# Optimization experiments

Measured on AMD Instinct MI355X. Metric: run time of the kernel, lower is better.

Reference implementation:

```python
import jax, jax.numpy as jnp
import numpy as np
from jax import lax

E = 4; D_MODEL = 128; D_FF = 128; DT_RANK = 32; D_STATE = 16
L = 12; PAD = 12  # padding_factor=1.0 -> pad L extra zeros
K_TOP = 6; U = 1e-6; EPS = 1e-5
BATCH = 8; NODES = 307; BN = BATCH * NODES
FREQ_IN = (L + PAD) // 2 + 1 + K_TOP  # 19
FREQ_OUT = L // 2 + 1                 # 7


def setup_inputs() -> dict:
    key = jax.random.key(0)
    ks = jax.random.split(key, 14)
    x = jax.random.normal(ks[0], (BN, L, D_MODEL), jnp.float32)
    graph = jax.random.normal(ks[1], (BATCH, L, D_FF, D_FF), jnp.float32) * (1.0 / D_FF)
    in_w = jax.random.normal(ks[2], (E, 2 * D_FF, D_MODEL), jnp.float32) * 0.05
    in_b = jax.random.normal(ks[3], (E, 2 * D_FF), jnp.float32) * 0.02
    x_w = jax.random.normal(ks[4], (E, DT_RANK + 2 * D_STATE + D_FF, D_FF), jnp.float32) * 0.05
    dt_w = jax.random.uniform(ks[5], (E, D_FF, DT_RANK), jnp.float32,
                              -(DT_RANK ** -0.5), DT_RANK ** -0.5)
    dt_b = -2.0 + 0.1 * jax.random.normal(ks[6], (E, D_FF), jnp.float32)
    A_log = jnp.broadcast_to(jnp.log(jnp.arange(1, D_STATE + 1, dtype=jnp.float32))[None, None, :],
                             (E, 1, D_STATE))
    out_w = jax.random.normal(ks[7], (E, D_MODEL, D_FF), jnp.float32) * 0.05
    out_b = jax.random.normal(ks[8], (E, D_MODEL), jnp.float32) * 0.02
    fw_r = jax.random.normal(ks[9], (E, FREQ_OUT, FREQ_IN), jnp.float32) * (FREQ_IN ** -0.5)
    fw_i = jax.random.normal(ks[10], (E, FREQ_OUT, FREQ_IN), jnp.float32) * (FREQ_IN ** -0.5)
    norm_w = jnp.ones((E, D_MODEL), jnp.float32)
    blk_w = jnp.full((E,), 0.5, jnp.float32)
    blk_b = jnp.full((E,), 0.5, jnp.float32)
    return dict(x=x, graph=graph, in_w=in_w, in_b=in_b, x_w=x_w, dt_w=dt_w, dt_b=dt_b,
                A_log=A_log, out_w=out_w, out_b=out_b, fw_r=fw_r, fw_i=fw_i,
                norm_w=norm_w, blk_w=blk_w, blk_b=blk_b)


def _rmsnorm(x, w):
    return x * lax.rsqrt(jnp.mean(x * x, axis=-1, keepdims=True) + EPS) * w


def _mamba_block(x, graph, in_w, in_b, x_w, dt_w, dt_b, A_log, out_w, out_b, fw_r, fw_i):
    bn, Ls, d = x.shape
    # --- FFT frequency gating ---
    x_padded = jnp.concatenate([x, jnp.zeros((bn, PAD, d), x.dtype)], axis=1)
    fp = jnp.fft.rfft(x_padded, axis=1)          # [bn, 13, d] complex
    f = jnp.fft.rfft(x, axis=1)                  # [bn, 7, d] complex
    sq_adj = (f.real + U) ** 2 + (f.imag + U) ** 2
    fs = -jnp.sort(-sq_adj, axis=1)[:, :K_TOP]   # top-K along freq dim, descending
    cat = jnp.concatenate([fp, fs.astype(fp.dtype)], axis=1)  # [bn, 19, d]
    W = lax.complex(fw_r, fw_i)                  # [7, 19]
    freq_proj = jnp.einsum('bkd,ok->bod', cat, W)  # [bn, 7, d]
    wf = jax.nn.softmax(freq_proj.real ** 2 + freq_proj.imag ** 2, axis=2)
    x_freq = jnp.fft.irfft(wf * f, axis=1)       # [bn, 12, d] (n = 2*(7-1))
    # --- input projection ---
    xz = x @ in_w.T + in_b
    xs, z = jnp.split(xz, 2, axis=-1)
    xs = jax.nn.silu(xs)
    # --- SSM ---
    A = -jnp.exp(A_log.astype(jnp.float32))      # [1, d_state]
    dbcd = xs @ x_w.T
    delta, B, C, Dp = jnp.split(dbcd, [DT_RANK, DT_RANK + D_STATE, DT_RANK + 2 * D_STATE], axis=-1)
    delta = jax.nn.softplus(delta @ dt_w.T + dt_b)  # [bn, L, d_ff]
    # graph mixing over nodes: bn = batch * n
    batch = graph.shape[0]
    delta = delta.reshape(batch, -1, Ls, D_FF)
    delta = jnp.einsum('bnsd,bsda->bnsa', delta, graph).reshape(bn, Ls, D_FF)
    deltaA = jnp.exp(delta[..., None] * A)             # [bn, L, d_ff, d_state]
    BX = delta[..., None] * B[:, :, None, :] * xs[..., None]
    dA_t = jnp.moveaxis(deltaA, 1, 0)
    bx_t = jnp.moveaxis(BX, 1, 0)

    def step(h, ab):
        dA, bx = ab
        h = dA * h + bx
        return h, h

    h0 = jnp.zeros((bn, D_FF, D_STATE), xs.dtype)
    _, hs = lax.scan(step, h0, (dA_t, bx_t))
    hs = jnp.moveaxis(hs, 0, 1)                        # [bn, L, d_ff, d_state]
    y = jnp.einsum('blds,bls->bld', hs, C) + Dp * xs
    # --- gate + output ---
    out = y * jax.nn.silu(z) * x_freq
    return out @ out_w.T + out_b


def reference(x, graph, in_w, in_b, x_w, dt_w, dt_b, A_log, out_w, out_b,
              fw_r, fw_i, norm_w, blk_w, blk_b):
    for i in range(E):
        xn = _rmsnorm(x, norm_w[i])
        out = _mamba_block(xn, graph, in_w[i], in_b[i], x_w[i], dt_w[i], dt_b[i],
                           A_log[i], out_w[i], out_b[i], fw_r[i], fw_i[i])
        out = blk_w[i] * out + blk_b[i]
        x = x + out  # dropout is identity in eval
    return jax.nn.silu(x)
```

## Files before the change

kernel.cpp:

```cpp
#include <hip/hip_runtime.h>
#include <math.h>

#define BN    2456
#define LSEQ  12
#define DM    128
#define NODES 307
#define MROWS 29472

typedef __bf16 bfx8 __attribute__((ext_vector_type(8)));
typedef float  f32x4 __attribute__((ext_vector_type(4)));

#define MFMA16(a, b, c) __builtin_amdgcn_mfma_f32_16x16x32_bf16(a, b, c, 0, 0, 0)

__device__ __forceinline__ float fsilu(float v)     { return v / (1.0f + __expf(-v)); }
__device__ __forceinline__ float fsoftplus(float x) { return fmaxf(x, 0.f) + __logf(1.0f + __expf(-fabsf(x))); }

__global__ __launch_bounds__(256)
void k_convert(const float* __restrict__ in_w, const float* __restrict__ x_w,
               const float* __restrict__ out_w, const float* __restrict__ dt_w,
               const float* __restrict__ graph,
               __bf16* __restrict__ in_w_bf, __bf16* __restrict__ x_w_bf,
               __bf16* __restrict__ out_w_bf, __bf16* __restrict__ dtw_bf,
               __bf16* __restrict__ graphT_bf) {
    int idx = blockIdx.x * 256 + threadIdx.x;
    if (idx < 131072) { in_w_bf[idx] = (__bf16)in_w[idx]; return; }
    idx -= 131072;
    if (idx < 98304) { x_w_bf[idx] = (__bf16)x_w[idx]; return; }
    idx -= 98304;
    if (idx < 65536) { out_w_bf[idx] = (__bf16)out_w[idx]; return; }
    idx -= 65536;
    if (idx < 65536) { dtw_bf[idx] = (__bf16)dt_w[idx]; return; }
    idx -= 65536;
    if (idx < 1572864) {
        int bl = idx >> 14, r = idx & 16383;
        int d = r >> 7, a = r & 127;
        graphT_bf[(size_t)bl * 16384 + a * 128 + d] = (__bf16)graph[idx];
    }
}

template <int N>
__device__ __forceinline__ void red_sum128(float* v, float* sred, int tid) {
#pragma unroll
    for (int off = 32; off; off >>= 1)
#pragma unroll
        for (int i = 0; i < N; ++i) v[i] += __shfl_xor(v[i], off, 64);
    if ((tid & 63) == 0) {
#pragma unroll
        for (int i = 0; i < N; ++i) sred[(tid >> 6) * N + i] = v[i];
    }
    __syncthreads();
#pragma unroll
    for (int i = 0; i < N; ++i) v[i] = sred[i] + sred[N + i];
    __syncthreads();
}

template <int N>
__device__ __forceinline__ void red_max128(float* v, float* sred, int tid) {
#pragma unroll
    for (int off = 32; off; off >>= 1)
#pragma unroll
        for (int i = 0; i < N; ++i) v[i] = fmaxf(v[i], __shfl_xor(v[i], off, 64));
    if ((tid & 63) == 0) {
#pragma unroll
        for (int i = 0; i < N; ++i) sred[(tid >> 6) * N + i] = v[i];
    }
    __syncthreads();
#pragma unroll
    for (int i = 0; i < N; ++i) v[i] = fmaxf(sred[i], sred[N + i]);
    __syncthreads();
}

__global__ __launch_bounds__(128)
void k_freq(const float* __restrict__ xcur, const float* __restrict__ norm_w,
            const float* __restrict__ fw_r, const float* __restrict__ fw_i,
            __bf16* __restrict__ xn_bf, __bf16* __restrict__ xfq_bf, int e) {
    __shared__ float s_c[24], s_s[24], s_wr[133], s_wi[133];
    __shared__ float sred[24];
    const int row = blockIdx.x, tid = threadIdx.x;
    const int b = row / NODES, n = row - b * NODES;

    if (tid < 24) {
        float sv, cv;
        __sincosf(6.283185307179586f * (float)tid / 24.0f, &sv, &cv);
        s_c[tid] = cv; s_s[tid] = sv;
    }
    for (int i = tid; i < 133; i += 128) { s_wr[i] = fw_r[e * 133 + i]; s_wi[i] = fw_i[e * 133 + i]; }

    const float* xp = xcur + (size_t)row * 1536 + tid;
    float xv[12], v[12];
#pragma unroll
    for (int l = 0; l < 12; ++l) { xv[l] = xp[l * 128]; v[l] = xv[l] * xv[l]; }
    __syncthreads();
    red_sum128<12>(v, sred, tid);

    const float nrmw = norm_w[e * DM + tid];
    float xnr[12];
#pragma unroll
    for (int l = 0; l < 12; ++l)
        xnr[l] = xv[l] * rsqrtf(v[l] * (1.0f / 128.0f) + 1e-5f) * nrmw;

#pragma unroll
    for (int l = 0; l < 12; ++l)
        xn_bf[((size_t)(b * 12 + l) * NODES + n) * 128 + tid] = (__bf16)xnr[l];

    float fpr[13], fpi[13];
#pragma unroll
    for (int k = 0; k < 13; ++k) { fpr[k] = 0.f; fpi[k] = 0.f; }
#pragma unroll
    for (int l = 0; l < 12; ++l) {
#pragma unroll
        for (int k = 0; k < 13; ++k) {
            const int t = (k * l) % 24;
            fpr[k] += xnr[l] * s_c[t];
            fpi[k] -= xnr[l] * s_s[t];
        }
    }

    float a7[7];
#pragma unroll
    for (int o2 = 0; o2 < 7; ++o2) {
        float ar = fpr[2 * o2] + 1e-6f, ai = fpi[2 * o2] + 1e-6f;
        a7[o2] = ar * ar + ai * ai;
    }
#pragma unroll
    for (int pss = 0; pss < 6; ++pss)
#pragma unroll
        for (int j = 0; j < 6; ++j) {
            float hi = fmaxf(a7[j], a7[j + 1]);
            float lo = fminf(a7[j], a7[j + 1]);
            a7[j] = hi; a7[j + 1] = lo;
        }

    float p7[7];
#pragma unroll
    for (int o2 = 0; o2 < 7; ++o2) {
        float pr = 0.f, pi = 0.f;
#pragma unroll
        for (int k = 0; k < 13; ++k) {
            const float wr = s_wr[o2 * 19 + k], wi = s_wi[o2 * 19 + k];
            pr += fpr[k] * wr - fpi[k] * wi;
            pi += fpr[k] * wi + fpi[k] * wr;
        }
#pragma unroll
        for (int k = 0; k < 6; ++k) {
            const float wr = s_wr[o2 * 19 + 13 + k], wi = s_wi[o2 * 19 + 13 + k];
            pr += a7[k] * wr;
            pi += a7[k] * wi;
        }
        p7[o2] = pr * pr + pi * pi;
    }

    float m7[7], ex[7], sm[7];
#pragma unroll
    for (int o2 = 0; o2 < 7; ++o2) m7[o2] = p7[o2];
    red_max128<7>(m7, sred, tid);
#pragma unroll
    for (int o2 = 0; o2 < 7; ++o2) { ex[o2] = __expf(p7[o2] - m7[o2]); sm[o2] = ex[o2]; }
    red_sum128<7>(sm, sred, tid);

    float gr[7], gi[7];
#pragma unroll
    for (int o2 = 0; o2 < 7; ++o2) {
        const float wf = ex[o2] / sm[o2];
        gr[o2] = wf * fpr[2 * o2];
        gi[o2] = wf * fpi[2 * o2];
    }

#pragma unroll
    for (int l = 0; l < 12; ++l) {
        float val = gr[0] + ((l & 1) ? -gr[6] : gr[6]);
#pragma unroll
        for (int o2 = 1; o2 < 6; ++o2) {
            const int t = (2 * o2 * l) % 24;
            val += 2.0f * (gr[o2] * s_c[t] - gi[o2] * s_s[t]);
        }
        xfq_bf[((size_t)(b * 12 + l) * NODES + n) * 128 + tid] = (__bf16)(val * (1.0f / 12.0f));
    }
}

__global__ __launch_bounds__(256)
void k_fused(const __bf16* __restrict__ xn_bf, const __bf16* __restrict__ in_w_bf,
             const float* __restrict__ in_b, const __bf16* __restrict__ x_w_bf,
             const __bf16* __restrict__ dtw_bf, const float* __restrict__ dt_b,
             const __bf16* __restrict__ graphT_bf,
             __bf16* __restrict__ xs_bf, __bf16* __restrict__ sz_bf,
             float* __restrict__ bcf32, __bf16* __restrict__ dpf,
             __bf16* __restrict__ dmix_bf, int e) {
    __shared__ __bf16 sxs[16 * 136];
    __shared__ __bf16 sdelta[16 * 136];
    __shared__ __bf16 sdel32[16 * 40];
    const int bl = blockIdx.x;
    const int n0 = blockIdx.y * 16;
    const int tid = threadIdx.x;
    const int wave = tid >> 6, lane = tid & 63;
    const int lm = lane & 15, lq = lane >> 4;
    const size_t rowbase = (size_t)bl * NODES + n0;

    const __bf16* Wi = in_w_bf + (size_t)e * 256 * 128;
    const size_t arow = (size_t)bl * NODES + min(n0 + lm, NODES - 1);
    bfx8 af[4];
#pragma unroll
    for (int kc = 0; kc < 4; ++kc)
        af[kc] = *(const bfx8*)(xn_bf + arow * 128 + kc * 32 + lq * 8);

    f32x4 acc[4];
#pragma unroll
    for (int nt = 0; nt < 4; ++nt) acc[nt] = (f32x4){0.f, 0.f, 0.f, 0.f};
#pragma unroll
    for (int kc = 0; kc < 4; ++kc) {
        const int kb = kc * 32 + lq * 8;
#pragma unroll
        for (int ntl = 0; ntl < 4; ++ntl) {
            bfx8 b = *(const bfx8*)(Wi + (size_t)(wave * 64 + ntl * 16 + lm) * 128 + kb);
            acc[ntl] = MFMA16(af[kc], b, acc[ntl]);
        }
    }
#pragma unroll
    for (int ntl = 0; ntl < 4; ++ntl) {
        const int col = wave * 64 + ntl * 16 + lm;
        const float bias = in_b[e * 256 + col];
#pragma unroll
        for (int r = 0; r < 4; ++r) {
            const int node = lq * 4 + r;
            const float v = fsilu(acc[ntl][r] + bias);
            const int ok = (n0 + node) < NODES;
            if (col < 128) {
                sxs[node * 136 + col] = (__bf16)v;
                if (ok) xs_bf[(rowbase + node) * 128 + col] = (__bf16)v;
            } else if (ok) {
                sz_bf[(rowbase + node) * 128 + (col - 128)] = (__bf16)v;
            }
        }
    }
    __syncthreads();

    const __bf16* Wx = x_w_bf + (size_t)e * 192 * 128;
    bfx8 ax[4];
#pragma unroll
    for (int kc = 0; kc < 4; ++kc)
        ax[kc] = *(const bfx8*)(sxs + lm * 136 + kc * 32 + lq * 8);

    f32x4 xacc[3];
#pragma unroll
    for (int nt = 0; nt < 3; ++nt) xacc[nt] = (f32x4){0.f, 0.f, 0.f, 0.f};
#pragma unroll
    for (int kc = 0; kc < 4; ++kc) {
        const int kb = kc * 32 + lq * 8;
#pragma unroll
        for (int ntl = 0; ntl < 3; ++ntl) {
            bfx8 b = *(const bfx8*)(Wx + (size_t)((wave * 3 + ntl) * 16 + lm) * 128 + kb);
            xacc[ntl] = MFMA16(ax[kc], b, xacc[ntl]);
        }
    }
#pragma unroll
    for (int ntl = 0; ntl < 3; ++ntl) {
        const int col = (wave * 3 + ntl) * 16 + lm;
#pragma unroll
        for (int r = 0; r < 4; ++r) {
            const int node = lq * 4 + r;
            const float v = xacc[ntl][r];
            const int ok = (n0 + node) < NODES;
            if (col < 32) sdel32[node * 40 + col] = (__bf16)v;
            else if (col < 64) { if (ok) bcf32[(rowbase + node) * 32 + (col - 32)] = v; }
            else if (ok) dpf[(rowbase + node) * 128 + (col - 64)] = (__bf16)v;
        }
    }
    __syncthreads();

    const __bf16* DW = dtw_bf + (size_t)e * 128 * 32;
    bfx8 ad = *(const bfx8*)(sdel32 + lm * 40 + lq * 8);
    const f32x4 z4 = {0.f, 0.f, 0.f, 0.f};
#pragma unroll
    for (int ntl = 0; ntl < 2; ++ntl) {
        const int nt = wave * 2 + ntl;
        bfx8 b = *(const bfx8*)(DW + (size_t)(nt * 16 + lm) * 32 + lq * 8);
        f32x4 dacc = MFMA16(ad, b, z4);
        const int col = nt * 16 + lm;
        const float bias = dt_b[e * 128 + col];
#pragma unroll
        for (int r = 0; r < 4; ++r) {
            const int node = lq * 4 + r;
            sdelta[node * 136 + col] = (__bf16)fsoftplus(dacc[r] + bias);
        }
    }
    __syncthreads();

    const __bf16* Gp = graphT_bf + (size_t)bl * 16384;
    bfx8 ag[4];
#pragma unroll
    for (int kc = 0; kc < 4; ++kc)
        ag[kc] = *(const bfx8*)(sdelta + lm * 136 + kc * 32 + lq * 8);

#pragma unroll
    for (int ntl = 0; ntl < 2; ++ntl) {
        const int nt = wave * 2 + ntl;
        f32x4 gacc = z4;
#pragma unroll
        for (int kc = 0; kc < 4; ++kc) {
            const int kb = kc * 32 + lq * 8;
            bfx8 b = *(const bfx8*)(Gp + (size_t)(nt * 16 + lm) * 128 + kb);
            gacc = MFMA16(ag[kc], b, gacc);
        }
        const int col = nt * 16 + lm;
#pragma unroll
        for (int r = 0; r < 4; ++r) {
            const int node = lq * 4 + r;
            if ((n0 + node) < NODES)
                dmix_bf[(rowbase + node) * 128 + col] = (__bf16)gacc[r];
        }
    }
}

__global__ __launch_bounds__(128)
void k_scanout(const __bf16* __restrict__ dmix_bf, const __bf16* __restrict__ xs_bf,
               const __bf16* __restrict__ sz_bf, const __bf16* __restrict__ xfq_bf,
               const float* __restrict__ bcf32, const __bf16* __restrict__ dpf,
               const float* __restrict__ A_log, const __bf16* __restrict__ out_w_bf,
               const float* __restrict__ out_b, const float* __restrict__ blk_w,
               const float* __restrict__ blk_b, const float* __restrict__ xprev,
               float* __restrict__ xout, int e, int last) {
    __shared__ __bf16 s_out[16 * 136];
    __shared__ float sBC[384];
    const int row = blockIdx.x, tid = threadIdx.x;
    const int b = row / NODES, n = row - b * NODES;
    for (int i = tid; i < 384; i += 128) {
        const int l = i >> 5, s = i & 31;
        sBC[i] = bcf32[((size_t)(b * 12 + l) * NODES + n) * 32 + s];
    }
    float As[16];
#pragma unroll
    for (int s = 0; s < 16; ++s) As[s] = -__expf(A_log[e * 16 + s]);
#pragma unroll
    for (int r = 12; r < 16; ++r) s_out[r * 136 + tid] = (__bf16)0.f;
    __syncthreads();

    float h[16];
#pragma unroll
    for (int s = 0; s < 16; ++s) h[s] = 0.f;
#pragma unroll
    for (int l = 0; l < 12; ++l) {
        const size_t base = ((size_t)(b * 12 + l) * NODES + n) * 128 + tid;
        const float dl = (float)dmix_bf[base];
        const float xv = (float)xs_bf[base];
        const float Dp = (float)dpf[base];
        const float dlx = dl * xv;
        float y = 0.f;
#pragma unroll
        for (int s = 0; s < 16; ++s) {
            h[s] = __expf(dl * As[s]) * h[s] + sBC[l * 32 + s] * dlx;
            y += h[s] * sBC[l * 32 + 16 + s];
        }
        y += Dp * xv;
        const float g = y * (float)sz_bf[base] * (float)xfq_bf[base];
        s_out[l * 136 + tid] = (__bf16)g;
    }
    __syncthreads();

    const int wave = tid >> 6, lane = tid & 63;
    const int lm = lane & 15, lq = lane >> 4;
    const __bf16* Wo = out_w_bf + (size_t)e * 16384;
    bfx8 a[4];
#pragma unroll
    for (int kc = 0; kc < 4; ++kc)
        a[kc] = *(const bfx8*)(s_out + lm * 136 + kc * 32 + lq * 8);

    f32x4 acc[4];
#pragma unroll
    for (int nt = 0; nt < 4; ++nt) acc[nt] = (f32x4){0.f, 0.f, 0.f, 0.f};
#pragma unroll
    for (int kc = 0; kc < 4; ++kc) {
        const int kb = kc * 32 + lq * 8;
#pragma unroll
        for (int nt = 0; nt < 4; ++nt) {
            bfx8 b = *(const bfx8*)(Wo + (size_t)(wave * 64 + nt * 16 + lm) * 128 + kb);
            acc[nt] = MFMA16(a[kc], b, acc[nt]);
        }
    }

    const float bw = blk_w[e], bb = blk_b[e];
#pragma unroll
    for (int nt = 0; nt < 4; ++nt) {
        const int col = wave * 64 + nt * 16 + lm;
        const float ob = out_b[e * 128 + col];
#pragma unroll
        for (int r = 0; r < 4; ++r) {
            const int m = lq * 4 + r;
            if (m < 12) {
                const size_t gi = ((size_t)row * 12 + m) * 128 + col;
                float v = bw * (acc[nt][r] + ob) + bb + xprev[gi];
                if (last) v = fsilu(v);
                xout[gi] = v;
            }
        }
    }
}

extern "C" void kernel_launch(void* const* d_in, const int* in_sizes, int n_in,
                              void* d_out, int out_size, void* d_ws, size_t ws_size,
                              hipStream_t stream) {
    (void)in_sizes; (void)n_in; (void)out_size; (void)ws_size;
    const float* x_in   = (const float*)d_in[0];
    const float* graph  = (const float*)d_in[1];
    const float* in_w   = (const float*)d_in[2];
    const float* in_b   = (const float*)d_in[3];
    const float* x_w    = (const float*)d_in[4];
    const float* dt_w   = (const float*)d_in[5];
    const float* dt_b   = (const float*)d_in[6];
    const float* A_log  = (const float*)d_in[7];
    const float* out_w  = (const float*)d_in[8];
    const float* out_b  = (const float*)d_in[9];
    const float* fw_r   = (const float*)d_in[10];
    const float* fw_i   = (const float*)d_in[11];
    const float* norm_w = (const float*)d_in[12];
    const float* blk_w  = (const float*)d_in[13];
    const float* blk_b  = (const float*)d_in[14];
    float* out = (float*)d_out;

    float* ws = (float*)d_ws;
    size_t o = 0;
    __bf16* in_w_bf   = (__bf16*)(ws + o); o += 131072 / 2;
    __bf16* x_w_bf    = (__bf16*)(ws + o); o += 98304 / 2;
    __bf16* out_w_bf  = (__bf16*)(ws + o); o += 65536 / 2;
    __bf16* dtw_bf    = (__bf16*)(ws + o); o += 65536 / 2;
    __bf16* graphT_bf = (__bf16*)(ws + o); o += 1572864 / 2;
    const size_t NE = (size_t)MROWS * 128;
    __bf16* xn_bf    = (__bf16*)(ws + o); o += NE / 2;
    __bf16* xfq_bf   = (__bf16*)(ws + o); o += NE / 2;
    __bf16* xs_bf    = (__bf16*)(ws + o); o += NE / 2;
    __bf16* sz_bf    = (__bf16*)(ws + o); o += NE / 2;
    __bf16* dpf      = (__bf16*)(ws + o); o += NE / 2;
    __bf16* dmix_bf  = (__bf16*)(ws + o); o += NE / 2;
    float*  bcf32    = ws + o;            o += (size_t)MROWS * 32;

    hipLaunchKernelGGL(k_convert, dim3(7552), dim3(256), 0, stream,
                       in_w, x_w, out_w, dt_w, graph,
                       in_w_bf, x_w_bf, out_w_bf, dtw_bf, graphT_bf);

    for (int e = 0; e < 4; ++e) {
        const float* xcur = (e == 0) ? x_in : (const float*)out;
        const int last = (e == 3) ? 1 : 0;
        hipLaunchKernelGGL(k_freq, dim3(BN), dim3(128), 0, stream,
                           xcur, norm_w, fw_r, fw_i, xn_bf, xfq_bf, e);
        hipLaunchKernelGGL(k_fused, dim3(96, 20), dim3(256), 0, stream,
                           xn_bf, in_w_bf, in_b, x_w_bf, dtw_bf, dt_b, graphT_bf,
                           xs_bf, sz_bf, bcf32, dpf, dmix_bf, e);
        hipLaunchKernelGGL(k_scanout, dim3(BN), dim3(128), 0, stream,
                           dmix_bf, xs_bf, sz_bf, xfq_bf, bcf32, dpf, A_log,
                           out_w_bf, out_b, blk_w, blk_b, xcur, out, e, last);
    }
}
```

Baseline: 465.4 us.

## Fuse RMSNorm and frequency gating into consumers and pre-swizzle weights into MFMA layout

Removes the separate k_freq kernel. RMSNorm is now computed inside k_fused straight from the fp32 activations. The FFT gating is recomputed inside k_scanout, so the xn and xfq bf16 intermediates are no longer written to or read from global memory. Weights and the graph are converted once into an MFMA-fragment-ordered layout, so each lane loads contiguous 16-byte fragments, and they are prefetched early in k_fused. The cost is more register pressure and duplicated RMSNorm work, since both kernels now read xcur in fp32.

```diff
diff --git a/kernel.cpp b/kernel.cpp
--- a/kernel.cpp
+++ b/kernel.cpp
@@ -17,24 +17,55 @@
 
 __global__ __launch_bounds__(256)
 void k_convert(const float* __restrict__ in_w, const float* __restrict__ x_w,
-               const float* __restrict__ out_w, const float* __restrict__ dt_w,
+               const float* __restrict__ dt_w, const float* __restrict__ out_w,
                const float* __restrict__ graph,
-               __bf16* __restrict__ in_w_bf, __bf16* __restrict__ x_w_bf,
-               __bf16* __restrict__ out_w_bf, __bf16* __restrict__ dtw_bf,
-               __bf16* __restrict__ graphT_bf) {
+               __bf16* __restrict__ in_w_sw, __bf16* __restrict__ x_w_sw,
+               __bf16* __restrict__ dtw_sw, __bf16* __restrict__ out_w_sw,
+               __bf16* __restrict__ graph_sw) {
     int idx = blockIdx.x * 256 + threadIdx.x;
-    if (idx < 131072) { in_w_bf[idx] = (__bf16)in_w[idx]; return; }
+    if (idx < 131072) {
+        int o = idx;
+        int e = o >> 15, r = o & 32767;
+        int frag = r >> 9, lane = (r >> 3) & 63, j = r & 7;
+        int nt = frag >> 2, kc = frag & 3, lm = lane & 15, lq = lane >> 4;
+        in_w_sw[o] = (__bf16)in_w[e * 32768 + (nt * 16 + lm) * 128 + kc * 32 + lq * 8 + j];
+        return;
+    }
     idx -= 131072;
-    if (idx < 98304) { x_w_bf[idx] = (__bf16)x_w[idx]; return; }
+    if (idx < 98304) {
+        int o = idx;
+        int e = o / 24576, r = o - e * 24576;
+        int frag = r >> 9, lane = (r >> 3) & 63, j = r & 7;
+        int nt = frag >> 2, kc = frag & 3, lm = lane & 15, lq = lane >> 4;
+        x_w_sw[o] = (__bf16)x_w[e * 24576 + (nt * 16 + lm) * 128 + kc * 32 + lq * 8 + j];
+        return;
+    }
     idx -= 98304;
-    if (idx < 65536) { out_w_bf[idx] = (__bf16)out_w[idx]; return; }
-    idx -= 65536;
-    if (idx < 65536) { dtw_bf[idx] = (__bf16)dt_w[idx]; return; }
+    if (idx < 16384) {
+        int o = idx;
+        int e = o >> 12, r = o & 4095;
+        int nt = r >> 9, lane = (r >> 3) & 63, j = r & 7;
+        int lm = lane & 15, lq = lane >> 4;
+        dtw_sw[o] = (__bf16)dt_w[e * 4096 + (nt * 16 + lm) * 32 + lq * 8 + j];
+        return;
+    }
+    idx -= 16384;
+    if (idx < 65536) {
+        int o = idx;
+        int e = o >> 14, r = o & 16383;
+        int frag = r >> 9, lane = (r >> 3) & 63, j = r & 7;
+        int f = frag >> 2, kc = frag & 3, lm = lane & 15, lq = lane >> 4;
+        out_w_sw[o] = (__bf16)out_w[e * 16384 + (f * 16 + lm) * 128 + kc * 32 + lq * 8 + j];
+        return;
+    }
     idx -= 65536;
     if (idx < 1572864) {
-        int bl = idx >> 14, r = idx & 16383;
-        int d = r >> 7, a = r & 127;
-        graphT_bf[(size_t)bl * 16384 + a * 128 + d] = (__bf16)graph[idx];
+        int o = idx;
+        int bl = o >> 14, r = o & 16383;
+        int frag = r >> 9, lane = (r >> 3) & 63, j = r & 7;
+        int nt = frag >> 2, kc = frag & 3, lm = lane & 15, lq = lane >> 4;
+        int a = nt * 16 + lm, d = kc * 32 + lq * 8 + j;
+        graph_sw[o] = (__bf16)graph[(size_t)bl * 16384 + d * 128 + a];
     }
 }
 
@@ -70,119 +101,11 @@
     __syncthreads();
 }
 
-__global__ __launch_bounds__(128)
-void k_freq(const float* __restrict__ xcur, const float* __restrict__ norm_w,
-            const float* __restrict__ fw_r, const float* __restrict__ fw_i,
-            __bf16* __restrict__ xn_bf, __bf16* __restrict__ xfq_bf, int e) {
-    __shared__ float s_c[24], s_s[24], s_wr[133], s_wi[133];
-    __shared__ float sred[24];
-    const int row = blockIdx.x, tid = threadIdx.x;
-    const int b = row / NODES, n = row - b * NODES;
-
-    if (tid < 24) {
-        float sv, cv;
-        __sincosf(6.283185307179586f * (float)tid / 24.0f, &sv, &cv);
-        s_c[tid] = cv; s_s[tid] = sv;
-    }
-    for (int i = tid; i < 133; i += 128) { s_wr[i] = fw_r[e * 133 + i]; s_wi[i] = fw_i[e * 133 + i]; }
-
-    const float* xp = xcur + (size_t)row * 1536 + tid;
-    float xv[12], v[12];
-#pragma unroll
-    for (int l = 0; l < 12; ++l) { xv[l] = xp[l * 128]; v[l] = xv[l] * xv[l]; }
-    __syncthreads();
-    red_sum128<12>(v, sred, tid);
-
-    const float nrmw = norm_w[e * DM + tid];
-    float xnr[12];
-#pragma unroll
-    for (int l = 0; l < 12; ++l)
-        xnr[l] = xv[l] * rsqrtf(v[l] * (1.0f / 128.0f) + 1e-5f) * nrmw;
-
-#pragma unroll
-    for (int l = 0; l < 12; ++l)
-        xn_bf[((size_t)(b * 12 + l) * NODES + n) * 128 + tid] = (__bf16)xnr[l];
-
-    float fpr[13], fpi[13];
-#pragma unroll
-    for (int k = 0; k < 13; ++k) { fpr[k] = 0.f; fpi[k] = 0.f; }
-#pragma unroll
-    for (int l = 0; l < 12; ++l) {
-#pragma unroll
-        for (int k = 0; k < 13; ++k) {
-            const int t = (k * l) % 24;
-            fpr[k] += xnr[l] * s_c[t];
-            fpi[k] -= xnr[l] * s_s[t];
-        }
-    }
-
-    float a7[7];
-#pragma unroll
-    for (int o2 = 0; o2 < 7; ++o2) {
-        float ar = fpr[2 * o2] + 1e-6f, ai = fpi[2 * o2] + 1e-6f;
-        a7[o2] = ar * ar + ai * ai;
-    }
-#pragma unroll
-    for (int pss = 0; pss < 6; ++pss)
-#pragma unroll
-        for (int j = 0; j < 6; ++j) {
-            float hi = fmaxf(a7[j], a7[j + 1]);
-            float lo = fminf(a7[j], a7[j + 1]);
-            a7[j] = hi; a7[j + 1] = lo;
-        }
-
-    float p7[7];
-#pragma unroll
-    for (int o2 = 0; o2 < 7; ++o2) {
-        float pr = 0.f, pi = 0.f;
-#pragma unroll
-        for (int k = 0; k < 13; ++k) {
-            const float wr = s_wr[o2 * 19 + k], wi = s_wi[o2 * 19 + k];
-            pr += fpr[k] * wr - fpi[k] * wi;
-            pi += fpr[k] * wi + fpi[k] * wr;
-        }
-#pragma unroll
-        for (int k = 0; k < 6; ++k) {
-            const float wr = s_wr[o2 * 19 + 13 + k], wi = s_wi[o2 * 19 + 13 + k];
-            pr += a7[k] * wr;
-            pi += a7[k] * wi;
-        }
-        p7[o2] = pr * pr + pi * pi;
-    }
-
-    float m7[7], ex[7], sm[7];
-#pragma unroll
-    for (int o2 = 0; o2 < 7; ++o2) m7[o2] = p7[o2];
-    red_max128<7>(m7, sred, tid);
-#pragma unroll
-    for (int o2 = 0; o2 < 7; ++o2) { ex[o2] = __expf(p7[o2] - m7[o2]); sm[o2] = ex[o2]; }
-    red_sum128<7>(sm, sred, tid);
-
-    float gr[7], gi[7];
-#pragma unroll
-    for (int o2 = 0; o2 < 7; ++o2) {
-        const float wf = ex[o2] / sm[o2];
-        gr[o2] = wf * fpr[2 * o2];
-        gi[o2] = wf * fpi[2 * o2];
-    }
-
-#pragma unroll
-    for (int l = 0; l < 12; ++l) {
-        float val = gr[0] + ((l & 1) ? -gr[6] : gr[6]);
-#pragma unroll
-        for (int o2 = 1; o2 < 6; ++o2) {
-            const int t = (2 * o2 * l) % 24;
-            val += 2.0f * (gr[o2] * s_c[t] - gi[o2] * s_s[t]);
-        }
-        xfq_bf[((size_t)(b * 12 + l) * NODES + n) * 128 + tid] = (__bf16)(val * (1.0f / 12.0f));
-    }
-}
-
 __global__ __launch_bounds__(256)
-void k_fused(const __bf16* __restrict__ xn_bf, const __bf16* __restrict__ in_w_bf,
-             const float* __restrict__ in_b, const __bf16* __restrict__ x_w_bf,
-             const __bf16* __restrict__ dtw_bf, const float* __restrict__ dt_b,
-             const __bf16* __restrict__ graphT_bf,
+void k_fused(const float* __restrict__ xcur, const float* __restrict__ norm_w,
+             const __bf16* __restrict__ WiSw, const float* __restrict__ in_b,
+             const __bf16* __restrict__ WxSw, const __bf16* __restrict__ DWSw,
+             const float* __restrict__ dt_b, const __bf16* __restrict__ GSw,
              __bf16* __restrict__ xs_bf, __bf16* __restrict__ sz_bf,
              float* __restrict__ bcf32, __bf16* __restrict__ dpf,
              __bf16* __restrict__ dmix_bf, int e) {
@@ -194,27 +117,79 @@
     const int tid = threadIdx.x;
     const int wave = tid >> 6, lane = tid & 63;
     const int lm = lane & 15, lq = lane >> 4;
+    const int b = bl / 12, l = bl - b * 12;
     const size_t rowbase = (size_t)bl * NODES + n0;
 
-    const __bf16* Wi = in_w_bf + (size_t)e * 256 * 128;
-    const size_t arow = (size_t)bl * NODES + min(n0 + lm, NODES - 1);
+    const int nodeA = min(n0 + lm, NODES - 1);
+    const float* xrow = xcur + ((size_t)(b * NODES + nodeA) * 12 + l) * 128 + lq * 8;
+    float xv[4][8];
+#pragma unroll
+    for (int kc = 0; kc < 4; ++kc) {
+        float4 p0 = *(const float4*)(xrow + kc * 32);
+        float4 p1 = *(const float4*)(xrow + kc * 32 + 4);
+        xv[kc][0] = p0.x; xv[kc][1] = p0.y; xv[kc][2] = p0.z; xv[kc][3] = p0.w;
+        xv[kc][4] = p1.x; xv[kc][5] = p1.y; xv[kc][6] = p1.z; xv[kc][7] = p1.w;
+    }
+    float ss = 0.f;
+#pragma unroll
+    for (int kc = 0; kc < 4; ++kc)
+#pragma unroll
+        for (int j = 0; j < 8; ++j) ss += xv[kc][j] * xv[kc][j];
+    ss += __shfl_xor(ss, 16, 64);
+    ss += __shfl_xor(ss, 32, 64);
+    const float rms = rsqrtf(ss * (1.0f / 128.0f) + 1e-5f);
+
     bfx8 af[4];
-#pragma unroll
-    for (int kc = 0; kc < 4; ++kc)
-        af[kc] = *(const bfx8*)(xn_bf + arow * 128 + kc * 32 + lq * 8);
-
+    const float* nwp = norm_w + e * DM + lq * 8;
+#pragma unroll
+    for (int kc = 0; kc < 4; ++kc) {
+        float4 w0 = *(const float4*)(nwp + kc * 32);
+        float4 w1 = *(const float4*)(nwp + kc * 32 + 4);
+        af[kc][0] = (__bf16)(xv[kc][0] * rms * w0.x);
+        af[kc][1] = (__bf16)(xv[kc][1] * rms * w0.y);
+        af[kc][2] = (__bf16)(xv[kc][2] * rms * w0.z);
+        af[kc][3] = (__bf16)(xv[kc][3] * rms * w0.w);
+        af[kc][4] = (__bf16)(xv[kc][4] * rms * w1.x);
+        af[kc][5] = (__bf16)(xv[kc][5] * rms * w1.y);
+        af[kc][6] = (__bf16)(xv[kc][6] * rms * w1.z);
+        af[kc][7] = (__bf16)(xv[kc][7] * rms * w1.w);
+    }
+
+    const __bf16* WxP = WxSw + (size_t)e * 24576;
+    bfx8 b2[3][4];
+#pragma unroll
+    for (int ntl = 0; ntl < 3; ++ntl)
+#pragma unroll
+        for (int kc = 0; kc < 4; ++kc)
+            b2[ntl][kc] = *(const bfx8*)(WxP + (((wave * 3 + ntl) * 4 + kc) * 64 + lane) * 8);
+
+    const __bf16* WiP = WiSw + (size_t)e * 32768;
     f32x4 acc[4];
 #pragma unroll
     for (int nt = 0; nt < 4; ++nt) acc[nt] = (f32x4){0.f, 0.f, 0.f, 0.f};
 #pragma unroll
-    for (int kc = 0; kc < 4; ++kc) {
-        const int kb = kc * 32 + lq * 8;
-#pragma unroll
-        for (int ntl = 0; ntl < 4; ++ntl) {
-            bfx8 b = *(const bfx8*)(Wi + (size_t)(wave * 64 + ntl * 16 + lm) * 128 + kb);
-            acc[ntl] = MFMA16(af[kc], b, acc[ntl]);
-        }
-    }
+    for (int ntl = 0; ntl < 4; ++ntl) {
+        const int nt = wave * 4 + ntl;
+#pragma unroll
+        for (int kc = 0; kc < 4; ++kc) {
+            bfx8 bb = *(const bfx8*)(WiP + ((nt * 4 + kc) * 64 + lane) * 8);
+            acc[ntl] = MFMA16(af[kc], bb, acc[ntl]);
+        }
+    }
+
+    const __bf16* DWp = DWSw + (size_t)e * 4096;
+    bfx8 b3[2];
+#pragma unroll
+    for (int ntl = 0; ntl < 2; ++ntl)
+        b3[ntl] = *(const bfx8*)(DWp + ((wave * 2 + ntl) * 64 + lane) * 8);
+    const __bf16* Gp = GSw + (size_t)bl * 16384;
+    bfx8 b4[2][4];
+#pragma unroll
+    for (int ntl = 0; ntl < 2; ++ntl)
+#pragma unroll
+        for (int kc = 0; kc < 4; ++kc)
+            b4[ntl][kc] = *(const bfx8*)(Gp + (((wave * 2 + ntl) * 4 + kc) * 64 + lane) * 8);
+
 #pragma unroll
     for (int ntl = 0; ntl < 4; ++ntl) {
         const int col = wave * 64 + ntl * 16 + lm;
@@ -234,7 +209,6 @@
     }
     __syncthreads();
 
-    const __bf16* Wx = x_w_bf + (size_t)e * 192 * 128;
     bfx8 ax[4];
 #pragma unroll
     for (int kc = 0; kc < 4; ++kc)
@@ -244,14 +218,11 @@
 #pragma unroll
     for (int nt = 0; nt < 3; ++nt) xacc[nt] = (f32x4){0.f, 0.f, 0.f, 0.f};
 #pragma unroll
-    for (int kc = 0; kc < 4; ++kc) {
-        const int kb = kc * 32 + lq * 8;
-#pragma unroll
-        for (int ntl = 0; ntl < 3; ++ntl) {
-            bfx8 b = *(const bfx8*)(Wx + (size_t)((wave * 3 + ntl) * 16 + lm) * 128 + kb);
-            xacc[ntl] = MFMA16(ax[kc], b, xacc[ntl]);
-        }
-    }
+    for (int ntl = 0; ntl < 3; ++ntl)
+#pragma unroll
+        for (int kc = 0; kc < 4; ++kc)
+            xacc[ntl] = MFMA16(ax[kc], b2[ntl][kc], xacc[ntl]);
+
 #pragma unroll
     for (int ntl = 0; ntl < 3; ++ntl) {
         const int col = (wave * 3 + ntl) * 16 + lm;
@@ -267,15 +238,12 @@
     }
     __syncthreads();
 
-    const __bf16* DW = dtw_bf + (size_t)e * 128 * 32;
     bfx8 ad = *(const bfx8*)(sdel32 + lm * 40 + lq * 8);
     const f32x4 z4 = {0.f, 0.f, 0.f, 0.f};
 #pragma unroll
     for (int ntl = 0; ntl < 2; ++ntl) {
-        const int nt = wave * 2 + ntl;
-        bfx8 b = *(const bfx8*)(DW + (size_t)(nt * 16 + lm) * 32 + lq * 8);
-        f32x4 dacc = MFMA16(ad, b, z4);
-        const int col = nt * 16 + lm;
+        f32x4 dacc = MFMA16(ad, b3[ntl], z4);
+        const int col = (wave * 2 + ntl) * 16 + lm;
         const float bias = dt_b[e * 128 + col];
 #pragma unroll
         for (int r = 0; r < 4; ++r) {
@@ -285,7 +253,6 @@
     }
     __syncthreads();
 
-    const __bf16* Gp = graphT_bf + (size_t)bl * 16384;
     bfx8 ag[4];
 #pragma unroll
     for (int kc = 0; kc < 4; ++kc)
@@ -293,15 +260,11 @@
 
 #pragma unroll
     for (int ntl = 0; ntl < 2; ++ntl) {
-        const int nt = wave * 2 + ntl;
         f32x4 gacc = z4;
 #pragma unroll
-        for (int kc = 0; kc < 4; ++kc) {
-            const int kb = kc * 32 + lq * 8;
-            bfx8 b = *(const bfx8*)(Gp + (size_t)(nt * 16 + lm) * 128 + kb);
-            gacc = MFMA16(ag[kc], b, gacc);
-        }
-        const int col = nt * 16 + lm;
+        for (int kc = 0; kc < 4; ++kc)
+            gacc = MFMA16(ag[kc], b4[ntl][kc], gacc);
+        const int col = (wave * 2 + ntl) * 16 + lm;
 #pragma unroll
         for (int r = 0; r < 4; ++r) {
             const int node = lq * 4 + r;
@@ -312,28 +275,133 @@
 }
 
 __global__ __launch_bounds__(128)
-void k_scanout(const __bf16* __restrict__ dmix_bf, const __bf16* __restrict__ xs_bf,
-               const __bf16* __restrict__ sz_bf, const __bf16* __restrict__ xfq_bf,
-               const float* __restrict__ bcf32, const __bf16* __restrict__ dpf,
-               const float* __restrict__ A_log, const __bf16* __restrict__ out_w_bf,
-               const float* __restrict__ out_b, const float* __restrict__ blk_w,
-               const float* __restrict__ blk_b, const float* __restrict__ xprev,
+void k_scanout(const float* __restrict__ xcur, const float* __restrict__ norm_w,
+               const float* __restrict__ fw_r, const float* __restrict__ fw_i,
+               const __bf16* __restrict__ dmix_bf, const __bf16* __restrict__ xs_bf,
+               const __bf16* __restrict__ sz_bf, const float* __restrict__ bcf32,
+               const __bf16* __restrict__ dpf, const float* __restrict__ A_log,
+               const __bf16* __restrict__ WoSw, const float* __restrict__ out_b,
+               const float* __restrict__ blk_w, const float* __restrict__ blk_b,
                float* __restrict__ xout, int e, int last) {
+    __shared__ float s_c[24], s_s[24], s_wr[133], s_wi[133];
+    __shared__ float sred[24];
     __shared__ __bf16 s_out[16 * 136];
     __shared__ float sBC[384];
     const int row = blockIdx.x, tid = threadIdx.x;
     const int b = row / NODES, n = row - b * NODES;
-    for (int i = tid; i < 384; i += 128) {
-        const int l = i >> 5, s = i & 31;
-        sBC[i] = bcf32[((size_t)(b * 12 + l) * NODES + n) * 32 + s];
-    }
+
+    float bcreg[3];
+#pragma unroll
+    for (int i = 0; i < 3; ++i) {
+        const int ii = tid + i * 128;
+        const int l = ii >> 5, s = ii & 31;
+        bcreg[i] = bcf32[((size_t)(b * 12 + l) * NODES + n) * 32 + s];
+    }
+
+    if (tid < 24) {
+        float sv, cv;
+        __sincosf(6.283185307179586f * (float)tid / 24.0f, &sv, &cv);
+        s_c[tid] = cv; s_s[tid] = sv;
+    }
+    for (int i = tid; i < 133; i += 128) { s_wr[i] = fw_r[e * 133 + i]; s_wi[i] = fw_i[e * 133 + i]; }
+
+    const float* xp = xcur + (size_t)row * 1536 + tid;
+    float xvf[12], v[12];
+#pragma unroll
+    for (int l = 0; l < 12; ++l) { xvf[l] = xp[l * 128]; v[l] = xvf[l] * xvf[l]; }
+    __syncthreads();
+    red_sum128<12>(v, sred, tid);
+
+    const float nrmw = norm_w[e * DM + tid];
+    float xnr[12];
+#pragma unroll
+    for (int l = 0; l < 12; ++l)
+        xnr[l] = xvf[l] * rsqrtf(v[l] * (1.0f / 128.0f) + 1e-5f) * nrmw;
+
+    float fpr[13], fpi[13];
+#pragma unroll
+    for (int k = 0; k < 13; ++k) { fpr[k] = 0.f; fpi[k] = 0.f; }
+#pragma unroll
+    for (int l = 0; l < 12; ++l) {
+#pragma unroll
+        for (int k = 0; k < 13; ++k) {
+            const int t = (k * l) % 24;
+            fpr[k] += xnr[l] * s_c[t];
+            fpi[k] -= xnr[l] * s_s[t];
+        }
+    }
+
+    float a7[7];
+#pragma unroll
+    for (int o2 = 0; o2 < 7; ++o2) {
+        float ar = fpr[2 * o2] + 1e-6f, ai = fpi[2 * o2] + 1e-6f;
+        a7[o2] = ar * ar + ai * ai;
+    }
+#pragma unroll
+    for (int pss = 0; pss < 6; ++pss)
+#pragma unroll
+        for (int j = 0; j < 6; ++j) {
+            float hi = fmaxf(a7[j], a7[j + 1]);
+            float lo = fminf(a7[j], a7[j + 1]);
+            a7[j] = hi; a7[j + 1] = lo;
+        }
+
+    float p7[7];
+#pragma unroll
+    for (int o2 = 0; o2 < 7; ++o2) {
+        float pr = 0.f, pi = 0.f;
+#pragma unroll
+        for (int k = 0; k < 13; ++k) {
+            const float wr = s_wr[o2 * 19 + k], wi = s_wi[o2 * 19 + k];
+            pr += fpr[k] * wr - fpi[k] * wi;
+            pi += fpr[k] * wi + fpi[k] * wr;
+        }
+#pragma unroll
+        for (int k = 0; k < 6; ++k) {
+            const float wr = s_wr[o2 * 19 + 13 + k], wi = s_wi[o2 * 19 + 13 + k];
+            pr += a7[k] * wr;
+            pi += a7[k] * wi;
+        }
+        p7[o2] = pr * pr + pi * pi;
+    }
+
+    float m7[7], ex[7], sm[7];
+#pragma unroll
+    for (int o2 = 0; o2 < 7; ++o2) m7[o2] = p7[o2];
+    red_max128<7>(m7, sred, tid);
+#pragma unroll
+    for (int o2 = 0; o2 < 7; ++o2) { ex[o2] = __expf(p7[o2] - m7[o2]); sm[o2] = ex[o2]; }
+    red_sum128<7>(sm, sred, tid);
+
+    float gr[7], gi[7];
+#pragma unroll
+    for (int o2 = 0; o2 < 7; ++o2) {
+        const float wf = ex[o2] / sm[o2];
+        gr[o2] = wf * fpr[2 * o2];
+        gi[o2] = wf * fpi[2 * o2];
+    }
+
+    float xfqv[12];
+#pragma unroll
+    for (int l = 0; l < 12; ++l) {
+        float val = gr[0] + ((l & 1) ? -gr[6] : gr[6]);
+#pragma unroll
+        for (int o2 = 1; o2 < 6; ++o2) {
+            const int t = (2 * o2 * l) % 24;
+            val += 2.0f * (gr[o2] * s_c[t] - gi[o2] * s_s[t]);
+        }
+        xfqv[l] = val * (1.0f / 12.0f);
+    }
+
+#pragma unroll
+    for (int i = 0; i < 3; ++i) sBC[tid + i * 128] = bcreg[i];
+#pragma unroll
+    for (int r = 12; r < 16; ++r) s_out[r * 136 + tid] = (__bf16)0.f;
+    __syncthreads();
+
     float As[16];
 #pragma unroll
     for (int s = 0; s < 16; ++s) As[s] = -__expf(A_log[e * 16 + s]);
-#pragma unroll
-    for (int r = 12; r < 16; ++r) s_out[r * 136 + tid] = (__bf16)0.f;
-    __syncthreads();
-
     float h[16];
 #pragma unroll
     for (int s = 0; s < 16; ++s) h[s] = 0.f;
@@ -341,24 +409,24 @@
     for (int l = 0; l < 12; ++l) {
         const size_t base = ((size_t)(b * 12 + l) * NODES + n) * 128 + tid;
         const float dl = (float)dmix_bf[base];
-        const float xv = (float)xs_bf[base];
+        const float xsv = (float)xs_bf[base];
         const float Dp = (float)dpf[base];
-        const float dlx = dl * xv;
+        const float dlx = dl * xsv;
         float y = 0.f;
 #pragma unroll
         for (int s = 0; s < 16; ++s) {
             h[s] = __expf(dl * As[s]) * h[s] + sBC[l * 32 + s] * dlx;
             y += h[s] * sBC[l * 32 + 16 + s];
         }
-        y += Dp * xv;
-        const float g = y * (float)sz_bf[base] * (float)xfq_bf[base];
+        y += Dp * xsv;
+        const float g = y * (float)sz_bf[base] * xfqv[l];
         s_out[l * 136 + tid] = (__bf16)g;
     }
     __syncthreads();
 
     const int wave = tid >> 6, lane = tid & 63;
     const int lm = lane & 15, lq = lane >> 4;
-    const __bf16* Wo = out_w_bf + (size_t)e * 16384;
+    const __bf16* Wop = WoSw + (size_t)e * 16384;
     bfx8 a[4];
 #pragma unroll
     for (int kc = 0; kc < 4; ++kc)
@@ -368,16 +436,16 @@
 #pragma unroll
     for (int nt = 0; nt < 4; ++nt) acc[nt] = (f32x4){0.f, 0.f, 0.f, 0.f};
 #pragma unroll
-    for (int kc = 0; kc < 4; ++kc) {
-        const int kb = kc * 32 + lq * 8;
-#pragma unroll
-        for (int nt = 0; nt < 4; ++nt) {
-            bfx8 b = *(const bfx8*)(Wo + (size_t)(wave * 64 + nt * 16 + lm) * 128 + kb);
-            acc[nt] = MFMA16(a[kc], b, acc[nt]);
-        }
-    }
-
-    const float bw = blk_w[e], bb = blk_b[e];
+    for (int nt = 0; nt < 4; ++nt) {
+        const int f = wave * 4 + nt;
+#pragma unroll
+        for (int kc = 0; kc < 4; ++kc) {
+            bfx8 bb = *(const bfx8*)(Wop + ((f * 4 + kc) * 64 + lane) * 8);
+            acc[nt] = MFMA16(a[kc], bb, acc[nt]);
+        }
+    }
+
+    const float bw = blk_w[e], bb2 = blk_b[e];
 #pragma unroll
     for (int nt = 0; nt < 4; ++nt) {
         const int col = wave * 64 + nt * 16 + lm;
@@ -387,9 +455,9 @@
             const int m = lq * 4 + r;
             if (m < 12) {
                 const size_t gi = ((size_t)row * 12 + m) * 128 + col;
-                float v = bw * (acc[nt][r] + ob) + bb + xprev[gi];
-                if (last) v = fsilu(v);
-                xout[gi] = v;
+                float vv = bw * (acc[nt][r] + ob) + bb2 + xcur[gi];
+                if (last) vv = fsilu(vv);
+                xout[gi] = vv;
             }
         }
     }
@@ -418,34 +486,30 @@
 
     float* ws = (float*)d_ws;
     size_t o = 0;
-    __bf16* in_w_bf   = (__bf16*)(ws + o); o += 131072 / 2;
-    __bf16* x_w_bf    = (__bf16*)(ws + o); o += 98304 / 2;
-    __bf16* out_w_bf  = (__bf16*)(ws + o); o += 65536 / 2;
-    __bf16* dtw_bf    = (__bf16*)(ws + o); o += 65536 / 2;
-    __bf16* graphT_bf = (__bf16*)(ws + o); o += 1572864 / 2;
+    __bf16* in_w_sw  = (__bf16*)(ws + o); o += 131072 / 2;
+    __bf16* x_w_sw   = (__bf16*)(ws + o); o += 98304 / 2;
+    __bf16* dtw_sw   = (__bf16*)(ws + o); o += 16384 / 2;
+    __bf16* out_w_sw = (__bf16*)(ws + o); o += 65536 / 2;
+    __bf16* graph_sw = (__bf16*)(ws + o); o += 1572864 / 2;
     const size_t NE = (size_t)MROWS * 128;
-    __bf16* xn_bf    = (__bf16*)(ws + o); o += NE / 2;
-    __bf16* xfq_bf   = (__bf16*)(ws + o); o += NE / 2;
     __bf16* xs_bf    = (__bf16*)(ws + o); o += NE / 2;
     __bf16* sz_bf    = (__bf16*)(ws + o); o += NE / 2;
     __bf16* dpf      = (__bf16*)(ws + o); o += NE / 2;
     __bf16* dmix_bf  = (__bf16*)(ws + o); o += NE / 2;
     float*  bcf32    = ws + o;            o += (size_t)MROWS * 32;
 
-    hipLaunchKernelGGL(k_convert, dim3(7552), dim3(256), 0, stream,
-                       in_w, x_w, out_w, dt_w, graph,
-                       in_w_bf, x_w_bf, out_w_bf, dtw_bf, graphT_bf);
+    hipLaunchKernelGGL(k_convert, dim3(7360), dim3(256), 0, stream,
+                       in_w, x_w, dt_w, out_w, graph,
+                       in_w_sw, x_w_sw, dtw_sw, out_w_sw, graph_sw);
 
     for (int e = 0; e < 4; ++e) {
         const float* xcur = (e == 0) ? x_in : (const float*)out;
         const int last = (e == 3) ? 1 : 0;
-        hipLaunchKernelGGL(k_freq, dim3(BN), dim3(128), 0, stream,
-                           xcur, norm_w, fw_r, fw_i, xn_bf, xfq_bf, e);
         hipLaunchKernelGGL(k_fused, dim3(96, 20), dim3(256), 0, stream,
-                           xn_bf, in_w_bf, in_b, x_w_bf, dtw_bf, dt_b, graphT_bf,
+                           xcur, norm_w, in_w_sw, in_b, x_w_sw, dtw_sw, dt_b, graph_sw,
                            xs_bf, sz_bf, bcf32, dpf, dmix_bf, e);
         hipLaunchKernelGGL(k_scanout, dim3(BN), dim3(128), 0, stream,
-                           dmix_bf, xs_bf, sz_bf, xfq_bf, bcf32, dpf, A_log,
-                           out_w_bf, out_b, blk_w, blk_b, xcur, out, e, last);
+                           xcur, norm_w, fw_r, fw_i, dmix_bf, xs_bf, sz_bf, bcf32,
+                           dpf, A_log, out_w_sw, out_b, blk_w, blk_b, out, e, last);
     }
 }
```

After: 407.9 us. 12.4% less time.
